# Kernel optimization log

Measured on AMD Instinct MI355X. Metric: run time of the kernel, lower is better.

The kernel has to match this reference:

```python
import jax, jax.numpy as jnp
import numpy as np

MASK_VALUE = -10000000.0

def reference(query, key, value, valid_length):
    # query: (B,n,d), key: (B,m,d), value: (B,m,dv), valid_length: (B,)
    d = key.shape[2]
    scale = 1.0 / jnp.sqrt(jnp.asarray(d, dtype=query.dtype))
    scores = jnp.einsum('bnd,bmd->bnm', query, key) * scale  # (B,n,m)
    m = key.shape[1]
    # mask positions >= valid_length per batch element
    mask = jnp.arange(m)[None, None, :] >= valid_length[:, None, None]  # (B,1,m)
    scores = jnp.where(mask, MASK_VALUE, scores)
    attn = jax.nn.softmax(scores, axis=-1)
    return jnp.einsum('bnm,bmv->bnv', attn, value)

def setup_inputs() -> dict:
    key = jax.random.key(0)
    k1, k2, k3, k4 = jax.random.split(key, 4)
    B, n, m, d, dv = 16, 1024, 1024, 128, 128
    return {
        'query': jax.random.normal(k1, (B, n, d), dtype=jnp.float32),
        'key': jax.random.normal(k2, (B, m, d), dtype=jnp.float32),
        'value': jax.random.normal(k3, (B, m, dv), dtype=jnp.float32),
        'valid_length': jax.random.randint(k4, (B,), 1, m + 1, dtype=jnp.int32),
    }
```

## Files before the change

### kernel.cpp

```cpp
#include <hip/hip_runtime.h>
#include <hip/hip_bf16.h>

typedef __attribute__((ext_vector_type(4))) float f32x4;
typedef __attribute__((ext_vector_type(8))) short s16x8;
typedef unsigned int u32;

#define DHEAD 128
#define KVB 32
#define BLKQ 64
#define NGRP 4
#define TILB 8192
#define LDSZ 131072

__device__ __forceinline__ short f2bf(float x) {
    __hip_bfloat16 h = __float2bfloat16(x);
    return *reinterpret_cast<short*>(&h);
}

__global__ __launch_bounds__(256)
void prep_frag(const float* __restrict__ K, const float* __restrict__ V,
               const int* __restrict__ VL,
               short* __restrict__ Kz, short* __restrict__ Vz, int m, int NT, int nkf) {
    const int i = blockIdx.x * 256 + threadIdx.x;
    if (i < nkf) {
        const int lane = i & 63;
        const int kk   = (i >> 6) & 3;
        const int s    = (i >> 8) & 1;
        const int rest = i >> 9;
        const int t = rest % NT, b = rest / NT;
        if (t * KVB >= VL[b]) return;
        const int qi = lane & 15, g = lane >> 4;
        const float* src = K + (size_t)(b * m + t * KVB + 16 * s + qi) * DHEAD + kk * 32 + g * 8;
        f32x4 a = *reinterpret_cast<const f32x4*>(src);
        f32x4 c = *reinterpret_cast<const f32x4*>(src + 4);
        s16x8 o;
        #pragma unroll
        for (int j = 0; j < 4; ++j) { o[j] = f2bf(a[j]); o[4 + j] = f2bf(c[j]); }
        *reinterpret_cast<s16x8*>(Kz + (size_t)i * 8) = o;
    } else {
        const int j = i - nkf;
        if (j < nkf) {
            const int lane = j & 63;
            const int dg   = (j >> 6) & 7;
            const int rest = j >> 9;
            const int t = rest % NT, b = rest / NT;
            if (t * KVB >= VL[b]) return;
            const int qi = lane & 15, g = lane >> 4;
            const float* vb = V + (size_t)(b * m + t * KVB + g * 4) * DHEAD + dg * 16 + qi;
            s16x8 o;
            #pragma unroll
            for (int r = 0; r < 4; ++r) {
                o[r]     = f2bf(vb[(size_t)r * DHEAD]);
                o[4 + r] = f2bf(vb[(size_t)(16 + r) * DHEAD]);
            }
            *reinterpret_cast<s16x8*>(Vz + (size_t)j * 8) = o;
        }
    }
}

__global__ __launch_bounds__(1024, 4)
void attn_fwd(const float* __restrict__ Q, const short* __restrict__ Kz,
              const short* __restrict__ Vz, const int* __restrict__ VL,
              float* __restrict__ O, int B, int n, int NT) {
    extern __shared__ char lds[];

    const int tid   = threadIdx.x;
    const int lane  = tid & 63;
    const int wid   = tid >> 6;
    const int qslot = wid & 3;
    const int grp   = wid >> 2;
    const int gl    = lane >> 4;
    const int qi    = lane & 15;

    const int nq = n / BLKQ;
    int b, qt;
    if ((B & 7) == 0) {
        const int xcd = blockIdx.x & 7;
        const int sub = blockIdx.x >> 3;
        const int bpx = B >> 3;
        b  = xcd * bpx + (sub % bpx);
        qt = sub / bpx;
    } else {
        b = blockIdx.x / nq; qt = blockIdx.x % nq;
    }

    const int vl = VL[b];
    const int nt = (vl + KVB - 1) / KVB;
    const int IT = (nt + NGRP - 1) / NGRP;
    const int rowbase = b * n + qt * BLKQ + qslot * 16;

    const float qsc = 0.08838834764831845f * 1.4426950408889634f;
    s16x8 qf[4];
    {
        const float* qp = Q + (size_t)(rowbase + qi) * DHEAD + gl * 8;
        #pragma unroll
        for (int kk = 0; kk < 4; ++kk) {
            f32x4 a  = *reinterpret_cast<const f32x4*>(qp + kk * 32);
            f32x4 cc = *reinterpret_cast<const f32x4*>(qp + kk * 32 + 4);
            s16x8 s;
            #pragma unroll
            for (int j = 0; j < 4; ++j) { s[j] = f2bf(a[j] * qsc); s[4 + j] = f2bf(cc[j] * qsc); }
            qf[kk] = s;
        }
    }

    const char* KzB = (const char*)Kz + (size_t)b * NT * TILB;
    const char* VzB = (const char*)Vz + (size_t)b * NT * TILB;

    auto DMA = [&](int buf, int t) {
        const char* ks = KzB + (size_t)t * TILB;
        const char* vs = VzB + (size_t)t * TILB;
        char* dst = &lds[grp * 32768 + buf * 16384];
        const int off = qslot * 2048;
        #pragma unroll
        for (int j = 0; j < 2; ++j) {
            __builtin_amdgcn_global_load_lds(
                (const __attribute__((address_space(1))) u32*)(ks + off + j * 1024 + lane * 16),
                (__attribute__((address_space(3))) u32*)(dst + off + j * 1024), 16, 0, 0);
            __builtin_amdgcn_global_load_lds(
                (const __attribute__((address_space(1))) u32*)(vs + off + j * 1024 + lane * 16),
                (__attribute__((address_space(3))) u32*)(dst + 8192 + off + j * 1024), 16, 0, 0);
        }
    };

    f32x4 Oacc[8];
    #pragma unroll
    for (int dg = 0; dg < 8; ++dg) Oacc[dg] = 0.f;
    float llocal = 0.f;
    const int lb = lane * 16;

    if (grp < nt) DMA(0, grp);
    __syncthreads();

    int cur = 0;
    #pragma unroll 1
    for (int i = 0; i < IT; ++i) {
        const int t  = grp + i * NGRP;
        const int tn = t + NGRP;
        if (tn < nt) DMA(cur ^ 1, tn);

        if (t < nt) {
            const char* ksb = &lds[grp * 32768 + cur * 16384];
            const char* vsb = ksb + 8192;

            f32x4 Sacc[2];
            Sacc[0] = 0.f; Sacc[1] = 0.f;
            __builtin_amdgcn_s_setprio(1);
            #pragma unroll
            for (int s = 0; s < 2; ++s)
                #pragma unroll
                for (int kk = 0; kk < 4; ++kk) {
                    s16x8 kf = *reinterpret_cast<const s16x8*>(ksb + (s * 4 + kk) * 1024 + lb);
                    Sacc[s] = __builtin_amdgcn_mfma_f32_16x16x32_bf16(kf, qf[kk], Sacc[s], 0, 0, 0);
                }
            __builtin_amdgcn_s_setprio(0);

            const int kvrem = vl - t * KVB;
            if (kvrem < KVB) {
                #pragma unroll
                for (int s = 0; s < 2; ++s)
                    #pragma unroll
                    for (int r = 0; r < 4; ++r)
                        if (s * 16 + gl * 4 + r >= kvrem) Sacc[s][r] = -1e30f;
            }

            s16x8 pa;
            #pragma unroll
            for (int s = 0; s < 2; ++s)
                #pragma unroll
                for (int r = 0; r < 4; ++r) {
                    const float e = __builtin_amdgcn_exp2f(fminf(Sacc[s][r], 60.f));
                    llocal += e;
                    pa[s * 4 + r] = f2bf(e);
                }

            __builtin_amdgcn_s_setprio(1);
            #pragma unroll
            for (int dg = 0; dg < 8; ++dg) {
                s16x8 vf = *reinterpret_cast<const s16x8*>(vsb + dg * 1024 + lb);
                Oacc[dg] = __builtin_amdgcn_mfma_f32_16x16x32_bf16(pa, vf, Oacc[dg], 0, 0, 0);
            }
            __builtin_amdgcn_s_setprio(0);
        }

        __syncthreads();
        cur ^= 1;
    }

    llocal += __shfl_xor(llocal, 16);
    llocal += __shfl_xor(llocal, 32);

    float* red  = (float*)lds;
    float* lred = (float*)&lds[98304];
    if (grp > 0) {
        float* w = red + (size_t)(grp - 1) * 8192 + qslot * 2048;
        #pragma unroll
        for (int dg = 0; dg < 8; ++dg)
            #pragma unroll
            for (int j = 0; j < 4; ++j)
                w[(gl * 4 + j) * 128 + dg * 16 + qi] = Oacc[dg][j];
        if (gl == 0) lred[(grp - 1) * 64 + qslot * 16 + qi] = llocal;
    }
    __syncthreads();

    if (grp == 0) {
        float ltot = llocal;
        #pragma unroll
        for (int g2 = 0; g2 < 3; ++g2) ltot += lred[g2 * 64 + qslot * 16 + qi];
        const float linv = 1.0f / ltot;
        const float l0 = __shfl(linv, gl * 4 + 0);
        const float l1 = __shfl(linv, gl * 4 + 1);
        const float l2 = __shfl(linv, gl * 4 + 2);
        const float l3 = __shfl(linv, gl * 4 + 3);
        float* Ob = O + (size_t)rowbase * DHEAD;
        #pragma unroll
        for (int dg = 0; dg < 8; ++dg) {
            float v0 = Oacc[dg][0], v1 = Oacc[dg][1], v2 = Oacc[dg][2], v3 = Oacc[dg][3];
            #pragma unroll
            for (int g2 = 0; g2 < 3; ++g2) {
                const float* rr = red + (size_t)g2 * 8192 + qslot * 2048;
                v0 += rr[(gl * 4 + 0) * 128 + dg * 16 + qi];
                v1 += rr[(gl * 4 + 1) * 128 + dg * 16 + qi];
                v2 += rr[(gl * 4 + 2) * 128 + dg * 16 + qi];
                v3 += rr[(gl * 4 + 3) * 128 + dg * 16 + qi];
            }
            Ob[(gl * 4 + 0) * DHEAD + dg * 16 + qi] = v0 * l0;
            Ob[(gl * 4 + 1) * DHEAD + dg * 16 + qi] = v1 * l1;
            Ob[(gl * 4 + 2) * DHEAD + dg * 16 + qi] = v2 * l2;
            Ob[(gl * 4 + 3) * DHEAD + dg * 16 + qi] = v3 * l3;
        }
    }
}

extern "C" void kernel_launch(void* const* d_in, const int* in_sizes, int n_in,
                              void* d_out, int out_size, void* d_ws, size_t ws_size,
                              hipStream_t stream) {
    const float* Q  = (const float*)d_in[0];
    const float* K  = (const float*)d_in[1];
    const float* V  = (const float*)d_in[2];
    const int*   VL = (const int*)d_in[3];
    float* O = (float*)d_out;

    const int B = in_sizes[3];
    const int n = in_sizes[0] / (B * DHEAD);
    const int m = in_sizes[1] / (B * DHEAD);
    const int NT = m / KVB;

    short* Kz = (short*)d_ws;
    short* Vz = Kz + (size_t)B * NT * (TILB / 2);

    const int nkf = B * NT * 512;
    prep_frag<<<(2 * nkf + 255) / 256, 256, 0, stream>>>(K, V, VL, Kz, Vz, m, NT, nkf);

    hipFuncSetAttribute((const void*)attn_fwd,
                        hipFuncAttributeMaxDynamicSharedMemorySize, LDSZ);
    const int grid = B * (n / BLKQ);
    attn_fwd<<<grid, 1024, LDSZ, stream>>>(Q, Kz, Vz, VL, O, B, n, NT);
}
```

Baseline: 26.54 us.

## Split KV range across blocks and add a combine kernel

```diff
diff --git a/kernel.cpp b/kernel.cpp
--- a/kernel.cpp
+++ b/kernel.cpp
@@ -9,12 +9,17 @@
 #define KVB 32
 #define BLKQ 64
 #define NGRP 4
+#define NSPL 2
 #define TILB 8192
 #define LDSZ 131072
 
 __device__ __forceinline__ short f2bf(float x) {
     __hip_bfloat16 h = __float2bfloat16(x);
     return *reinterpret_cast<short*>(&h);
+}
+__device__ __forceinline__ float bf2f(short s) {
+    __hip_bfloat16 h = *reinterpret_cast<__hip_bfloat16*>(&s);
+    return __bfloat162float(h);
 }
 
 __global__ __launch_bounds__(256)
@@ -61,7 +66,8 @@
 __global__ __launch_bounds__(1024, 4)
 void attn_fwd(const float* __restrict__ Q, const short* __restrict__ Kz,
               const short* __restrict__ Vz, const int* __restrict__ VL,
-              float* __restrict__ O, int B, int n, int NT) {
+              float* __restrict__ O, short* __restrict__ OPb, float* __restrict__ Lp,
+              int B, int n, int NT, int S, int rows) {
     extern __shared__ char lds[];
 
     const int tid   = threadIdx.x;
@@ -73,21 +79,31 @@
     const int qi    = lane & 15;
 
     const int nq = n / BLKQ;
-    int b, qt;
+    int b, rest;
     if ((B & 7) == 0) {
         const int xcd = blockIdx.x & 7;
         const int sub = blockIdx.x >> 3;
         const int bpx = B >> 3;
-        b  = xcd * bpx + (sub % bpx);
-        qt = sub / bpx;
+        b    = xcd * bpx + (sub % bpx);
+        rest = sub / bpx;
     } else {
-        b = blockIdx.x / nq; qt = blockIdx.x % nq;
-    }
+        const int per = nq * S;
+        b    = blockIdx.x / per;
+        rest = blockIdx.x % per;
+    }
+    const int qt = rest / S;
+    const int c  = rest % S;
 
     const int vl = VL[b];
     const int nt = (vl + KVB - 1) / KVB;
-    const int IT = (nt + NGRP - 1) / NGRP;
     const int rowbase = b * n + qt * BLKQ + qslot * 16;
+
+    if (c >= nt) {
+        if (S > 1 && grp == 0 && gl == 0) Lp[(size_t)c * rows + rowbase + qi] = 0.f;
+        return;
+    }
+    const int ntc = (nt - c + S - 1) / S;
+    const int IT  = (ntc + NGRP - 1) / NGRP;
 
     const float qsc = 0.08838834764831845f * 1.4426950408889634f;
     s16x8 qf[4];
@@ -123,20 +139,22 @@
         }
     };
 
+    auto TILE = [&](int i) { return c + S * (grp + NGRP * i); };
+
     f32x4 Oacc[8];
     #pragma unroll
     for (int dg = 0; dg < 8; ++dg) Oacc[dg] = 0.f;
     float llocal = 0.f;
     const int lb = lane * 16;
 
-    if (grp < nt) DMA(0, grp);
+    if (TILE(0) < nt) DMA(0, TILE(0));
     __syncthreads();
 
     int cur = 0;
     #pragma unroll 1
     for (int i = 0; i < IT; ++i) {
-        const int t  = grp + i * NGRP;
-        const int tn = t + NGRP;
+        const int t  = TILE(i);
+        const int tn = TILE(i + 1);
         if (tn < nt) DMA(cur ^ 1, tn);
 
         if (t < nt) {
@@ -207,29 +225,67 @@
         float ltot = llocal;
         #pragma unroll
         for (int g2 = 0; g2 < 3; ++g2) ltot += lred[g2 * 64 + qslot * 16 + qi];
-        const float linv = 1.0f / ltot;
-        const float l0 = __shfl(linv, gl * 4 + 0);
-        const float l1 = __shfl(linv, gl * 4 + 1);
-        const float l2 = __shfl(linv, gl * 4 + 2);
-        const float l3 = __shfl(linv, gl * 4 + 3);
-        float* Ob = O + (size_t)rowbase * DHEAD;
-        #pragma unroll
-        for (int dg = 0; dg < 8; ++dg) {
-            float v0 = Oacc[dg][0], v1 = Oacc[dg][1], v2 = Oacc[dg][2], v3 = Oacc[dg][3];
-            #pragma unroll
-            for (int g2 = 0; g2 < 3; ++g2) {
-                const float* rr = red + (size_t)g2 * 8192 + qslot * 2048;
-                v0 += rr[(gl * 4 + 0) * 128 + dg * 16 + qi];
-                v1 += rr[(gl * 4 + 1) * 128 + dg * 16 + qi];
-                v2 += rr[(gl * 4 + 2) * 128 + dg * 16 + qi];
-                v3 += rr[(gl * 4 + 3) * 128 + dg * 16 + qi];
-            }
-            Ob[(gl * 4 + 0) * DHEAD + dg * 16 + qi] = v0 * l0;
-            Ob[(gl * 4 + 1) * DHEAD + dg * 16 + qi] = v1 * l1;
-            Ob[(gl * 4 + 2) * DHEAD + dg * 16 + qi] = v2 * l2;
-            Ob[(gl * 4 + 3) * DHEAD + dg * 16 + qi] = v3 * l3;
-        }
-    }
+
+        if (S > 1) {
+            if (gl == 0) Lp[(size_t)c * rows + rowbase + qi] = ltot;
+            short* Op = OPb + ((size_t)c * rows + rowbase) * DHEAD;
+            #pragma unroll
+            for (int dg = 0; dg < 8; ++dg) {
+                float v[4];
+                #pragma unroll
+                for (int j = 0; j < 4; ++j) v[j] = Oacc[dg][j];
+                #pragma unroll
+                for (int g2 = 0; g2 < 3; ++g2) {
+                    const float* rr = red + (size_t)g2 * 8192 + qslot * 2048;
+                    #pragma unroll
+                    for (int j = 0; j < 4; ++j)
+                        v[j] += rr[(gl * 4 + j) * 128 + dg * 16 + qi];
+                }
+                #pragma unroll
+                for (int j = 0; j < 4; ++j)
+                    Op[(gl * 4 + j) * DHEAD + dg * 16 + qi] = f2bf(v[j]);
+            }
+        } else {
+            const float linv = 1.0f / ltot;
+            const float l0 = __shfl(linv, gl * 4 + 0);
+            const float l1 = __shfl(linv, gl * 4 + 1);
+            const float l2 = __shfl(linv, gl * 4 + 2);
+            const float l3 = __shfl(linv, gl * 4 + 3);
+            float* Ob = O + (size_t)rowbase * DHEAD;
+            #pragma unroll
+            for (int dg = 0; dg < 8; ++dg) {
+                float v0 = Oacc[dg][0], v1 = Oacc[dg][1], v2 = Oacc[dg][2], v3 = Oacc[dg][3];
+                #pragma unroll
+                for (int g2 = 0; g2 < 3; ++g2) {
+                    const float* rr = red + (size_t)g2 * 8192 + qslot * 2048;
+                    v0 += rr[(gl * 4 + 0) * 128 + dg * 16 + qi];
+                    v1 += rr[(gl * 4 + 1) * 128 + dg * 16 + qi];
+                    v2 += rr[(gl * 4 + 2) * 128 + dg * 16 + qi];
+                    v3 += rr[(gl * 4 + 3) * 128 + dg * 16 + qi];
+                }
+                Ob[(gl * 4 + 0) * DHEAD + dg * 16 + qi] = v0 * l0;
+                Ob[(gl * 4 + 1) * DHEAD + dg * 16 + qi] = v1 * l1;
+                Ob[(gl * 4 + 2) * DHEAD + dg * 16 + qi] = v2 * l2;
+                Ob[(gl * 4 + 3) * DHEAD + dg * 16 + qi] = v3 * l3;
+            }
+        }
+    }
+}
+
+__global__ __launch_bounds__(128)
+void attn_combine(const short* __restrict__ OPb, const float* __restrict__ Lp,
+                  float* __restrict__ O, int S, int rows) {
+    const int row = blockIdx.x;
+    const int t   = threadIdx.x;
+    float L = 0.f, acc = 0.f;
+    for (int s = 0; s < S; ++s) {
+        const float ls = Lp[(size_t)s * rows + row];
+        if (ls > 0.f) {
+            L += ls;
+            acc += bf2f(OPb[((size_t)s * rows + row) * DHEAD + t]);
+        }
+    }
+    O[(size_t)row * DHEAD + t] = acc / L;
 }
 
 extern "C" void kernel_launch(void* const* d_in, const int* in_sizes, int n_in,
@@ -244,16 +300,26 @@
     const int B = in_sizes[3];
     const int n = in_sizes[0] / (B * DHEAD);
     const int m = in_sizes[1] / (B * DHEAD);
+    const int rows = B * n;
     const int NT = m / KVB;
 
     short* Kz = (short*)d_ws;
     short* Vz = Kz + (size_t)B * NT * (TILB / 2);
+    const size_t used = 2 * (size_t)B * NT * TILB;
+
+    const size_t per_chunk = (size_t)rows * (DHEAD * 2 + 4);
+    const int S = (ws_size >= used + NSPL * per_chunk) ? NSPL : 1;
+
+    short* OPb = (short*)((char*)d_ws + used);
+    float* Lp  = (float*)((char*)d_ws + used + (size_t)S * rows * DHEAD * 2);
 
     const int nkf = B * NT * 512;
     prep_frag<<<(2 * nkf + 255) / 256, 256, 0, stream>>>(K, V, VL, Kz, Vz, m, NT, nkf);
 
     hipFuncSetAttribute((const void*)attn_fwd,
                         hipFuncAttributeMaxDynamicSharedMemorySize, LDSZ);
-    const int grid = B * (n / BLKQ);
-    attn_fwd<<<grid, 1024, LDSZ, stream>>>(Q, Kz, Vz, VL, O, B, n, NT);
-}
+    const int grid = B * (n / BLKQ) * S;
+    attn_fwd<<<grid, 1024, LDSZ, stream>>>(Q, Kz, Vz, VL, O, OPb, Lp, B, n, NT, S, rows);
+    if (S > 1)
+        attn_combine<<<rows, 128, 0, stream>>>(OPb, Lp, O, S, rows);
+}
```

Measured after the change: 42.84 us. 61.4% more time.
